# Kernel optimization log

Measured on AMD Instinct MI355X. Metric: run time of the kernel, lower is better.

The kernel has to match this reference:

```python
import jax, jax.numpy as jnp
import numpy as np

B, DV, W, H = 128, 2048, 14, 14
S = W * H            # 196 spatial positions
DQ = 2048            # question vector dim
DA = 1200            # attention dim_v == dim_q == dim_mm (MLB elementwise fusion)
G = 4                # nb_glimpses
DH = 2048            # fusion dim_h (total); per-glimpse = DH // G
NANS = 3000


def setup_inputs() -> dict:
    key = jax.random.key(0)
    ks = jax.random.split(key, 16)
    s = 0.02
    return {
        "input_v": jax.random.normal(ks[0], (B, DV, W, H), jnp.float32),
        "x_q_vec": jax.random.normal(ks[1], (B, DQ), jnp.float32),
        # conv_v_att: 1x1 conv DV->DA  (expressed as channel matmul)
        "Wv_att": jax.random.normal(ks[2], (DV, DA), jnp.float32) * s,
        "bv_att": jnp.zeros((DA,), jnp.float32),
        # linear_q_att: DQ->DA
        "Wq_att": jax.random.normal(ks[3], (DQ, DA), jnp.float32) * s,
        "bq_att": jnp.zeros((DA,), jnp.float32),
        # conv_att: 1x1 conv DA->G
        "Wa": jax.random.normal(ks[4], (DA, G), jnp.float32) * s,
        "ba": jnp.zeros((G,), jnp.float32),
        # per-glimpse fusion linears DV -> DH//G, stacked over glimpses
        "Wf": jax.random.normal(ks[5], (G, DV, DH // G), jnp.float32) * s,
        "bf": jnp.zeros((G, DH // G), jnp.float32),
        # linear_q_fusion: DQ -> DH
        "Wqf": jax.random.normal(ks[6], (DQ, DH), jnp.float32) * s,
        "bqf": jnp.zeros((DH,), jnp.float32),
        # linear_classif: DH -> NANS
        "Wc": jax.random.normal(ks[7], (DH, NANS), jnp.float32) * s,
        "bc": jnp.zeros((NANS,), jnp.float32),
    }


def reference(input_v, x_q_vec, Wv_att, bv_att, Wq_att, bq_att, Wa, ba,
              Wf, bf, Wqf, bqf, Wc, bc):
    b = input_v.shape[0]
    v_flat = input_v.reshape(b, DV, S)                      # [B, DV, S]

    # --- attention scores ---
    # conv_v_att (1x1) + tanh -> [B, S, DA]
    x_v = jnp.tanh(jnp.einsum('bcs,cd->bsd', v_flat, Wv_att) + bv_att)
    # linear_q_att + tanh -> [B, DA], broadcast over spatial
    x_q = jnp.tanh(x_q_vec @ Wq_att + bq_att)
    # MLB fusion_att: elementwise multiply, then tanh (activation_mm)
    x_att = jnp.tanh(x_v * x_q[:, None, :])                 # [B, S, DA]
    scores = jnp.einsum('bsd,dg->bsg', x_att, Wa) + ba      # [B, S, G]
    att = jax.nn.softmax(scores, axis=1)                    # softmax over spatial

    # --- weighted pooling per glimpse ---
    v_att = jnp.einsum('bsg,bcs->bgc', att, v_flat)         # [B, G, DV]

    # --- fusion of glimpses ---
    xv = jnp.tanh(jnp.einsum('bgc,gch->bgh', v_att, Wf) + bf)  # [B, G, DH/G]
    xv = xv.reshape(b, DH)                                   # concat glimpses
    xq = jnp.tanh(x_q_vec @ Wqf + bqf)                       # [B, DH]
    x = xv * xq                                              # MLB fusion_classif

    # --- classifier ---
    x = jnp.tanh(x)
    return x @ Wc + bc                                       # [B, NANS]
```

## Files before the change

### kernel.cpp

```cpp
#include <hip/hip_runtime.h>
#include <hip/hip_bf16.h>

#define BB   128
#define DV   2048
#define SS   196
#define DQ   2048
#define DA   1200
#define DAP  1280
#define GG   4
#define DH   2048
#define NANS 3000
#define NANSP 3008
#define MROWS (BB*SS)
#define NT   5
#define KSPLIT 8
#define KCHUNK (DV/KSPLIT)
#define NQ   (DAP + DH)

typedef __attribute__((ext_vector_type(8))) short bf16x8;
typedef __attribute__((ext_vector_type(4))) float f32x4;

__device__ __forceinline__ float fast_tanh(float x) {
    float e = __expf(2.0f * x);
    return 1.0f - 2.0f * __builtin_amdgcn_rcpf(e + 1.0f);
}

__device__ __forceinline__ void async_copy16(const void* gsrc, void* ldst) {
    __builtin_amdgcn_global_load_lds(
        (const __attribute__((address_space(1))) void*)gsrc,
        (__attribute__((address_space(3))) void*)ldst, 16, 0, 0);
}

__global__ void pad_misc(const float* __restrict__ bv, const float* __restrict__ Wa,
                         float* __restrict__ bvp, float* __restrict__ wap) {
    int i = blockIdx.x * 256 + threadIdx.x;
    if (i < DAP) bvp[i] = (i < DA) ? bv[i] : 0.f;
    if (i < DAP * GG) {
        int d = i >> 2;
        wap[i] = (d < DA) ? Wa[i] : 0.f;
    }
}

__global__ __launch_bounds__(256) void transpose_v(const float* __restrict__ v,
                                                   __hip_bfloat16* __restrict__ vt) {
    const int b    = blockIdx.z;
    const int t    = threadIdx.x;
    const int lane = t & 63;
    const int w    = t >> 6;
    const int sl   = lane >> 2;
    const int cq   = lane & 3;
    const int s    = blockIdx.y * 16 + sl;
    const int c0   = blockIdx.x * 128 + w * 32 + cq * 8;
    if (s >= SS) return;
    const float* src = v + (size_t)b * DV * SS + (size_t)c0 * SS + s;
    float f[8];
#pragma unroll
    for (int i = 0; i < 8; ++i) f[i] = src[(size_t)i * SS];
    union { bf16x8 v8; __hip_bfloat16 h[8]; } u;
#pragma unroll
    for (int i = 0; i < 8; ++i) u.h[i] = __float2bfloat16(f[i]);
    *(bf16x8*)(vt + ((size_t)b * SS + s) * DV + c0) = u.v8;
}

__global__ __launch_bounds__(256) void transpose_w(const float* __restrict__ Wv,
                                                   __hip_bfloat16* __restrict__ wvt) {
    __shared__ float tile[64][65];
    const int d0 = blockIdx.x * 64;
    const int c0 = blockIdx.y * 64;
    const int t  = threadIdx.x;
    const int col  = t & 63;
    const int rowb = t >> 6;
#pragma unroll
    for (int i = 0; i < 16; ++i) {
        int c = rowb + i * 4;
        int d = d0 + col;
        tile[c][col] = (d < DA) ? Wv[(size_t)(c0 + c) * DA + d] : 0.f;
    }
    __syncthreads();
#pragma unroll
    for (int i = 0; i < 16; ++i) {
        int dl = rowb + i * 4;
        wvt[(size_t)(d0 + dl) * DV + c0 + col] = __float2bfloat16(tile[col][dl]);
    }
}

template <int SEL>
__global__ __launch_bounds__(256) void gemm_partial(
    const float* __restrict__ A, int lda,
    const float* __restrict__ Bm, const float* __restrict__ B2,
    float* __restrict__ Cp, int Npad) {
    __shared__ float As[64 * 132];
    __shared__ float Bs[64 * 68];
    const int t     = threadIdx.x;
    const int n0    = blockIdx.x * 64;
    const int kbase = blockIdx.y * KCHUNK;

    const float* Aeff = A;
    const float* Beff;
    int ldb, ncol0, nlim;
    if (SEL == 0) {
        Beff = Bm; ldb = NANS; ncol0 = n0; nlim = NANS;
    } else if (SEL == 1) {
        int gg = n0 >> 9;
        Aeff = A + gg * 2048;
        Beff = Bm + (size_t)gg * 2048 * 512;
        ldb = 512; ncol0 = n0 & 511; nlim = 1 << 30;
    } else {
        if (n0 < DAP) { Beff = Bm; ldb = DA; ncol0 = n0;      nlim = DA; }
        else          { Beff = B2; ldb = DH; ncol0 = n0 - DAP; nlim = 1 << 30; }
    }

    const int tm = (t & 31) * 4;
    const int tn = (t >> 5) * 8;
    float acc[4][8] = {};

    for (int k0 = kbase; k0 < kbase + KCHUNK; k0 += 64) {
        {
            int kk = t & 63, mb = (t >> 6) * 32;
#pragma unroll
            for (int i = 0; i < 32; ++i)
                As[kk * 132 + mb + i] = Aeff[(size_t)(mb + i) * lda + k0 + kk];
        }
        {
            int j = t & 63, kr = t >> 6;
            bool ok = (ncol0 + j) < nlim;
#pragma unroll
            for (int i = 0; i < 16; ++i) {
                int k = kr + i * 4;
                Bs[k * 68 + j] = ok ? Beff[(size_t)(k0 + k) * ldb + ncol0 + j] : 0.f;
            }
        }
        __syncthreads();
#pragma unroll
        for (int kk = 0; kk < 64; ++kk) {
            const float4 av = *(const float4*)(As + kk * 132 + tm);
            const float4 b0 = *(const float4*)(Bs + kk * 68 + tn);
            const float4 b1 = *(const float4*)(Bs + kk * 68 + tn + 4);
            const float am[4] = {av.x, av.y, av.z, av.w};
#pragma unroll
            for (int i = 0; i < 4; ++i) {
                acc[i][0] += am[i] * b0.x; acc[i][1] += am[i] * b0.y;
                acc[i][2] += am[i] * b0.z; acc[i][3] += am[i] * b0.w;
                acc[i][4] += am[i] * b1.x; acc[i][5] += am[i] * b1.y;
                acc[i][6] += am[i] * b1.z; acc[i][7] += am[i] * b1.w;
            }
        }
        __syncthreads();
    }
#pragma unroll
    for (int i = 0; i < 4; ++i) {
        size_t base = ((size_t)blockIdx.y * 128 + tm + i) * Npad + n0 + tn;
        float4 v0 = {acc[i][0], acc[i][1], acc[i][2], acc[i][3]};
        float4 v1 = {acc[i][4], acc[i][5], acc[i][6], acc[i][7]};
        *(float4*)(Cp + base) = v0;
        *(float4*)(Cp + base + 4) = v1;
    }
}

template <int MODE>
__global__ __launch_bounds__(256) void gemm_epilogue(
    const float* __restrict__ Cp, int Npad, int Nreal,
    const float* __restrict__ bias, const float* __restrict__ aux,
    float* __restrict__ out, int ldo) {
    int n = blockIdx.x * 256 + threadIdx.x;
    int m = blockIdx.y;
    if (n >= Npad) return;
    float s = 0.f;
#pragma unroll
    for (int ks = 0; ks < KSPLIT; ++ks)
        s += Cp[((size_t)ks * 128 + m) * Npad + n];
    if (MODE == 0) {
        if (n >= Nreal) return;
        out[(size_t)m * ldo + n] = s + bias[n];
    } else {
        float xv = fast_tanh(s + bias[n]);
        out[(size_t)m * ldo + n] = fast_tanh(xv * aux[(size_t)m * 2048 + n]);
    }
}

__global__ __launch_bounds__(256) void epilogue_q(
    const float* __restrict__ Cp,
    const float* __restrict__ bqa, const float* __restrict__ bqf,
    float* __restrict__ qatt, float* __restrict__ qfus) {
    int n = blockIdx.x * 256 + threadIdx.x;
    int m = blockIdx.y;
    if (n >= NQ) return;
    float s = 0.f;
#pragma unroll
    for (int ks = 0; ks < KSPLIT; ++ks)
        s += Cp[((size_t)ks * 128 + m) * NQ + n];
    if (n < DAP) {
        qatt[(size_t)m * DAP + n] = (n < DA) ? fast_tanh(s + bqa[n]) : 0.f;
    } else {
        int j = n - DAP;
        qfus[(size_t)m * DH + j] = fast_tanh(s + bqf[j]);
    }
}

__global__ __launch_bounds__(512, 2) void big_gemm(
    const __hip_bfloat16* __restrict__ vt,
    const __hip_bfloat16* __restrict__ wt,
    const float* __restrict__ bvp,
    const float* __restrict__ qatt,
    const float* __restrict__ wap,
    float* __restrict__ scores_p) {
    __shared__ __align__(16) char lds[131072];
    __shared__ __align__(16) float wa_s[256 * 4];
    __shared__ float qs[3 * 256];

    const int t    = threadIdx.x;
    const int lane = t & 63;
    const int w    = t >> 6;
    const int wr   = w >> 2;
    const int wc   = w & 3;

    int bid = blockIdx.x;
    int grp = bid / 40, r = bid % 40;
    int mt, nt;
    if (grp < 12) { mt = grp * 8 + (r & 7); nt = r >> 3; }
    else          { mt = 96 + (r & 1);      nt = r >> 1; }
    const int m0 = mt * 256, n0 = nt * 256;
    const int b_lo = m0 / SS;
    const int bs1  = (b_lo + 1) * SS;
    const int bs2  = (b_lo + 2) * SS;

    if (t < 256) *(float4*)(wa_s + t * 4) = *(const float4*)(wap + (n0 + t) * 4);
    {
        int j = t >> 8, c = t & 255;
        int b = b_lo + j;
        qs[t] = (b < BB) ? qatt[(size_t)b * DAP + n0 + c] : 0.f;
        if (t < 256) {
            int b2 = b_lo + 2;
            qs[512 + t] = (b2 < BB) ? qatt[(size_t)b2 * DAP + n0 + t] : 0.f;
        }
    }
    __syncthreads();

    const int srow   = t >> 2;
    const int schunk = (t & 3) ^ ((t >> 3) & 3);
    const __hip_bfloat16* aG = vt + (size_t)(m0 + srow) * DV + schunk * 8;
    const __hip_bfloat16* bG = wt + (size_t)(n0 + srow) * DV + schunk * 8;

    auto STAGE_ITEM = [&](int buf, int k, int p) {
        const int ks = p >> 1, mat = p & 1;
        const __hip_bfloat16* g = (mat ? bG : aG) + (size_t)k * 64 + ks * 32;
        char* dst = lds + buf * 65536 + ks * 32768 + mat * 16384 + t * 16;
        async_copy16(g, dst);
        async_copy16(g + (size_t)128 * DV, dst + 8192);
    };

    const int rchk = ((lane >> 4) ^ (((lane & 15) >> 1) & 3)) * 16;
    const int aRow = (wr * 128 + (lane & 15)) * 64;
    const int bRow = (wc * 64 + (lane & 15)) * 64;

    f32x4 acc[8][4];
#pragma unroll
    for (int i = 0; i < 8; ++i)
#pragma unroll
        for (int j = 0; j < 4; ++j) acc[i][j] = (f32x4){0.f, 0.f, 0.f, 0.f};

    STAGE_ITEM(0, 0, 0); STAGE_ITEM(0, 0, 1);
    STAGE_ITEM(0, 0, 2); STAGE_ITEM(0, 0, 3);
    asm volatile("s_waitcnt vmcnt(4)" ::: "memory");
    __builtin_amdgcn_s_barrier();

    for (int kt = 0; kt < 32; ++kt) {
        const int cur = kt & 1;
        const char* Xb = lds + cur * 65536;
        bf16x8 bfr[4];
#pragma unroll
        for (int p = 0; p < 4; ++p) {
            const int ks = p >> 1, mh = p & 1;
            const char* Ar = Xb + ks * 32768;
            bf16x8 afr[4];
#pragma unroll
            for (int q = 0; q < 4; ++q)
                afr[q] = *(const bf16x8*)(Ar + aRow + (mh * 64 + q * 16) * 64 + rchk);
            if (mh == 0) {
#pragma unroll
                for (int ni = 0; ni < 4; ++ni)
                    bfr[ni] = *(const bf16x8*)(Ar + 16384 + bRow + (ni * 16) * 64 + rchk);
            }
            if (kt < 31) STAGE_ITEM(cur ^ 1, kt + 1, p);
            if (p == 1) {
                if (kt < 31) asm volatile("s_waitcnt vmcnt(4)" ::: "memory");
                else         asm volatile("s_waitcnt vmcnt(0)" ::: "memory");
            } else if (p == 3 && kt < 31) {
                asm volatile("s_waitcnt vmcnt(4)" ::: "memory");
            }
            __builtin_amdgcn_s_barrier();
            __builtin_amdgcn_s_setprio(1);
#pragma unroll
            for (int q = 0; q < 4; ++q)
#pragma unroll
                for (int ni = 0; ni < 4; ++ni)
                    acc[mh * 4 + q][ni] = __builtin_amdgcn_mfma_f32_16x16x32_bf16(
                        afr[q], bfr[ni], acc[mh * 4 + q][ni], 0, 0, 0);
            __builtin_amdgcn_s_setprio(0);
        }
    }

    __syncthreads();
    float* sc = (float*)lds;

    const int colb_l = wc * 64 + (lane & 15);
    const int colb_g = n0 + colb_l;
    float bvv[4];
    float4 wv[4];
#pragma unroll
    for (int ni = 0; ni < 4; ++ni) {
        bvv[ni] = bvp[colb_g + ni * 16];
        wv[ni]  = *(const float4*)(wa_s + (colb_l + ni * 16) * 4);
    }
#pragma unroll
    for (int mi = 0; mi < 8; ++mi) {
#pragma unroll
        for (int rr = 0; rr < 4; ++rr) {
            int lrow = wr * 128 + mi * 16 + ((lane >> 4) << 2) + rr;
            int row  = m0 + lrow;
            int qoff = (row >= bs1 ? 256 : 0) + (row >= bs2 ? 256 : 0);
            float p0 = 0.f, p1 = 0.f, p2 = 0.f, p3 = 0.f;
#pragma unroll
            for (int ni = 0; ni < 4; ++ni) {
                float xv = fast_tanh(acc[mi][ni][rr] + bvv[ni]);
                float xa = fast_tanh(xv * qs[qoff + colb_l + ni * 16]);
                p0 += xa * wv[ni].x; p1 += xa * wv[ni].y;
                p2 += xa * wv[ni].z; p3 += xa * wv[ni].w;
            }
#pragma unroll
            for (int mk = 1; mk < 16; mk <<= 1) {
                p0 += __shfl_xor(p0, mk); p1 += __shfl_xor(p1, mk);
                p2 += __shfl_xor(p2, mk); p3 += __shfl_xor(p3, mk);
            }
            if ((lane & 15) == 0)
                *(float4*)(sc + ((size_t)wc * 256 + lrow) * 4) =
                    (float4){p0, p1, p2, p3};
        }
    }
    __syncthreads();
    if (t < 256) {
        float4 s0 = *(float4*)(sc + (0 * 256 + t) * 4);
        float4 s1 = *(float4*)(sc + (1 * 256 + t) * 4);
        float4 s2 = *(float4*)(sc + (2 * 256 + t) * 4);
        float4 s3 = *(float4*)(sc + (3 * 256 + t) * 4);
        float4 s = {s0.x + s1.x + s2.x + s3.x, s0.y + s1.y + s2.y + s3.y,
                    s0.z + s1.z + s2.z + s3.z, s0.w + s1.w + s2.w + s3.w};
        *(float4*)(scores_p + ((size_t)nt * MROWS + m0 + t) * 4) = s;
    }
}

__global__ __launch_bounds__(256) void softmax_pool(
    const float* __restrict__ scores_p,
    const __hip_bfloat16* __restrict__ vt,
    float* __restrict__ vatt) {
    __shared__ __align__(16) float att[SS * GG];
    const int b = blockIdx.y;
    const int t = threadIdx.x;
    if (t < SS) {
        float4 s = {0.f, 0.f, 0.f, 0.f};
#pragma unroll
        for (int ntile = 0; ntile < NT; ++ntile) {
            float4 p = *(const float4*)(scores_p + ((size_t)ntile * MROWS + b * SS + t) * 4);
            s.x += p.x; s.y += p.y; s.z += p.z; s.w += p.w;
        }
        *(float4*)(att + t * 4) = s;
    }
    __syncthreads();
    {
        const int g = t >> 6;
        const int lane = t & 63;
        float mx = -3.0e38f;
        for (int s = lane; s < SS; s += 64) mx = fmaxf(mx, att[s * 4 + g]);
#pragma unroll
        for (int m = 32; m > 0; m >>= 1) mx = fmaxf(mx, __shfl_xor(mx, m));
        float sum = 0.f;
        for (int s = lane; s < SS; s += 64) sum += __expf(att[s * 4 + g] - mx);
#pragma unroll
        for (int m = 32; m > 0; m >>= 1) sum += __shfl_xor(sum, m);
        float inv = __builtin_amdgcn_rcpf(sum);
        for (int s = lane; s < SS; s += 64) att[s * 4 + g] = __expf(att[s * 4 + g] - mx) * inv;
    }
    __syncthreads();
    const int c = blockIdx.x * 512 + t * 2;
    const __hip_bfloat16* vp = vt + (size_t)b * SS * DV + c;
    float a00 = 0, a01 = 0, a02 = 0, a03 = 0;
    float a10 = 0, a11 = 0, a12 = 0, a13 = 0;
#pragma unroll 4
    for (int s = 0; s < SS; ++s) {
        unsigned u = *(const unsigned*)(vp + (size_t)s * DV);
        float v0 = __uint_as_float(u << 16);
        float v1 = __uint_as_float(u & 0xffff0000u);
        float4 aw = *(const float4*)(att + s * 4);
        a00 += v0 * aw.x; a01 += v0 * aw.y; a02 += v0 * aw.z; a03 += v0 * aw.w;
        a10 += v1 * aw.x; a11 += v1 * aw.y; a12 += v1 * aw.z; a13 += v1 * aw.w;
    }
    float* vb = vatt + (size_t)b * GG * DV;
    vb[0 * DV + c] = a00; vb[0 * DV + c + 1] = a10;
    vb[1 * DV + c] = a01; vb[1 * DV + c + 1] = a11;
    vb[2 * DV + c] = a02; vb[2 * DV + c + 1] = a12;
    vb[3 * DV + c] = a03; vb[3 * DV + c + 1] = a13;
}

extern "C" void kernel_launch(void* const* d_in, const int* in_sizes, int n_in,
                              void* d_out, int out_size, void* d_ws, size_t ws_size,
                              hipStream_t stream) {
    const float* input_v = (const float*)d_in[0];
    const float* x_q     = (const float*)d_in[1];
    const float* Wv      = (const float*)d_in[2];
    const float* bv      = (const float*)d_in[3];
    const float* Wq_att  = (const float*)d_in[4];
    const float* bq_att  = (const float*)d_in[5];
    const float* Wa      = (const float*)d_in[6];
    const float* Wf      = (const float*)d_in[8];
    const float* bf_     = (const float*)d_in[9];
    const float* Wqf     = (const float*)d_in[10];
    const float* bqf     = (const float*)d_in[11];
    const float* Wc      = (const float*)d_in[12];
    const float* bc      = (const float*)d_in[13];
    float* out = (float*)d_out;

    char* wsb = (char*)d_ws;
    size_t off = 0;
    auto carve = [&](size_t bytes) -> void* {
        void* p = wsb + off;
        off += (bytes + 255) & ~(size_t)255;
        return p;
    };
    __hip_bfloat16* vt  = (__hip_bfloat16*)carve((size_t)MROWS * DV * 2);
    __hip_bfloat16* wvt = (__hip_bfloat16*)carve((size_t)DAP * DV * 2);
    float* Cp       = (float*)carve((size_t)KSPLIT * 128 * NQ * 4);
    float* scores_p = (float*)carve((size_t)NT * MROWS * GG * 4);
    float* qatt = (float*)carve((size_t)BB * DAP * 4);
    float* qfus = (float*)carve((size_t)BB * DH * 4);
    float* bvp  = (float*)carve((size_t)DAP * 4);
    float* wap  = (float*)carve((size_t)DAP * GG * 4);
    float* vatt = (float*)carve((size_t)BB * GG * DV * 4);
    float* xbuf = (float*)carve((size_t)BB * DH * 4);
    (void)ws_size; (void)n_in; (void)in_sizes; (void)out_size;

    pad_misc<<<dim3(20), 256, 0, stream>>>(bv, Wa, bvp, wap);
    transpose_v<<<dim3(DV / 128, 13, BB), 256, 0, stream>>>(input_v, vt);
    transpose_w<<<dim3(DAP / 64, DV / 64), 256, 0, stream>>>(Wv, wvt);

    gemm_partial<2><<<dim3(NQ / 64, KSPLIT), 256, 0, stream>>>(
        x_q, DQ, Wq_att, Wqf, Cp, NQ);
    epilogue_q<<<dim3(NQ / 256, BB), 256, 0, stream>>>(Cp, bq_att, bqf, qatt, qfus);

    big_gemm<<<dim3(490), 512, 0, stream>>>(vt, wvt, bvp, qatt, wap, scores_p);

    softmax_pool<<<dim3(4, BB), 256, 0, stream>>>(scores_p, vt, vatt);

    gemm_partial<1><<<dim3(DH / 64, KSPLIT), 256, 0, stream>>>(
        vatt, GG * DV, Wf, nullptr, Cp, DH);
    gemm_epilogue<2><<<dim3(DH / 256, BB), 256, 0, stream>>>(
        Cp, DH, DH, bf_, qfus, xbuf, DH);

    gemm_partial<0><<<dim3(NANSP / 64, KSPLIT), 256, 0, stream>>>(
        xbuf, DH, Wc, nullptr, Cp, NANSP);
    gemm_epilogue<0><<<dim3(NANSP / 256 + 1, BB), 256, 0, stream>>>(
        Cp, NANSP, NANS, bc, nullptr, out, NANS);
}
```

Baseline: 646.0 us.

## Restructure big GEMM k-loop to two barriers per tile; widen pooling loads

The main GEMM inner loop now works through two k-substeps per tile instead of four phases. Each substep issues two staging loads up front, loads B fragments once, and runs two MFMA batches over the M halves. This halves the number of barriers and waitcnts per k-tile, with a sched_barrier to order the second A-fragment load. Separately, the softmax/pooling kernel has each thread handle four channels with 8-byte loads and float4 stores, on half as many blocks, which reduces parallelism in that kernel.

```diff
diff --git a/kernel.cpp b/kernel.cpp
--- a/kernel.cpp
+++ b/kernel.cpp
@@ -267,36 +267,44 @@
     for (int kt = 0; kt < 32; ++kt) {
         const int cur = kt & 1;
         const char* Xb = lds + cur * 65536;
-        bf16x8 bfr[4];
-#pragma unroll
-        for (int p = 0; p < 4; ++p) {
-            const int ks = p >> 1, mh = p & 1;
+#pragma unroll
+        for (int ks = 0; ks < 2; ++ks) {
             const char* Ar = Xb + ks * 32768;
-            bf16x8 afr[4];
+            if (kt < 31) {
+                STAGE_ITEM(cur ^ 1, kt + 1, 2 * ks);
+                STAGE_ITEM(cur ^ 1, kt + 1, 2 * ks + 1);
+            }
+            bf16x8 bfr[4], afr[4];
+#pragma unroll
+            for (int ni = 0; ni < 4; ++ni)
+                bfr[ni] = *(const bf16x8*)(Ar + 16384 + bRow + (ni * 16) * 64 + rchk);
 #pragma unroll
             for (int q = 0; q < 4; ++q)
-                afr[q] = *(const bf16x8*)(Ar + aRow + (mh * 64 + q * 16) * 64 + rchk);
-            if (mh == 0) {
+                afr[q] = *(const bf16x8*)(Ar + aRow + (q * 16) * 64 + rchk);
+            __builtin_amdgcn_s_setprio(1);
+#pragma unroll
+            for (int q = 0; q < 4; ++q)
 #pragma unroll
                 for (int ni = 0; ni < 4; ++ni)
-                    bfr[ni] = *(const bf16x8*)(Ar + 16384 + bRow + (ni * 16) * 64 + rchk);
-            }
-            if (kt < 31) STAGE_ITEM(cur ^ 1, kt + 1, p);
-            if (p == 1) {
-                if (kt < 31) asm volatile("s_waitcnt vmcnt(4)" ::: "memory");
-                else         asm volatile("s_waitcnt vmcnt(0)" ::: "memory");
-            } else if (p == 3 && kt < 31) {
-                asm volatile("s_waitcnt vmcnt(4)" ::: "memory");
-            }
+                    acc[q][ni] = __builtin_amdgcn_mfma_f32_16x16x32_bf16(
+                        afr[q], bfr[ni], acc[q][ni], 0, 0, 0);
+            __builtin_amdgcn_s_setprio(0);
+            __builtin_amdgcn_sched_barrier(0x8);
+            bf16x8 af2[4];
+#pragma unroll
+            for (int q = 0; q < 4; ++q)
+                af2[q] = *(const bf16x8*)(Ar + aRow + ((4 + q) * 16) * 64 + rchk);
+            __builtin_amdgcn_s_setprio(1);
+#pragma unroll
+            for (int q = 0; q < 4; ++q)
+#pragma unroll
+                for (int ni = 0; ni < 4; ++ni)
+                    acc[4 + q][ni] = __builtin_amdgcn_mfma_f32_16x16x32_bf16(
+                        af2[q], bfr[ni], acc[4 + q][ni], 0, 0, 0);
+            __builtin_amdgcn_s_setprio(0);
+            if (kt < 31) asm volatile("s_waitcnt vmcnt(4)" ::: "memory");
+            else         asm volatile("s_waitcnt vmcnt(0)" ::: "memory");
             __builtin_amdgcn_s_barrier();
-            __builtin_amdgcn_s_setprio(1);
-#pragma unroll
-            for (int q = 0; q < 4; ++q)
-#pragma unroll
-                for (int ni = 0; ni < 4; ++ni)
-                    acc[mh * 4 + q][ni] = __builtin_amdgcn_mfma_f32_16x16x32_bf16(
-                        afr[q], bfr[ni], acc[mh * 4 + q][ni], 0, 0, 0);
-            __builtin_amdgcn_s_setprio(0);
         }
     }
 
@@ -381,24 +389,28 @@
         for (int s = lane; s < SS; s += 64) att[s * 4 + g] = __expf(att[s * 4 + g] - mx) * inv;
     }
     __syncthreads();
-    const int c = blockIdx.x * 512 + t * 2;
+    const int c = blockIdx.x * 1024 + t * 4;
     const __hip_bfloat16* vp = vt + (size_t)b * SS * DV + c;
-    float a00 = 0, a01 = 0, a02 = 0, a03 = 0;
-    float a10 = 0, a11 = 0, a12 = 0, a13 = 0;
+    float a0[4] = {}, a1[4] = {}, a2[4] = {}, a3[4] = {};
 #pragma unroll 4
     for (int s = 0; s < SS; ++s) {
-        unsigned u = *(const unsigned*)(vp + (size_t)s * DV);
-        float v0 = __uint_as_float(u << 16);
-        float v1 = __uint_as_float(u & 0xffff0000u);
+        uint2 u = *(const uint2*)(vp + (size_t)s * DV);
+        float v0 = __uint_as_float(u.x << 16);
+        float v1 = __uint_as_float(u.x & 0xffff0000u);
+        float v2 = __uint_as_float(u.y << 16);
+        float v3 = __uint_as_float(u.y & 0xffff0000u);
         float4 aw = *(const float4*)(att + s * 4);
-        a00 += v0 * aw.x; a01 += v0 * aw.y; a02 += v0 * aw.z; a03 += v0 * aw.w;
-        a10 += v1 * aw.x; a11 += v1 * aw.y; a12 += v1 * aw.z; a13 += v1 * aw.w;
+        a0[0] += v0 * aw.x; a0[1] += v0 * aw.y; a0[2] += v0 * aw.z; a0[3] += v0 * aw.w;
+        a1[0] += v1 * aw.x; a1[1] += v1 * aw.y; a1[2] += v1 * aw.z; a1[3] += v1 * aw.w;
+        a2[0] += v2 * aw.x; a2[1] += v2 * aw.y; a2[2] += v2 * aw.z; a2[3] += v2 * aw.w;
+        a3[0] += v3 * aw.x; a3[1] += v3 * aw.y; a3[2] += v3 * aw.z; a3[3] += v3 * aw.w;
     }
     float* vb = vatt + (size_t)b * GG * DV;
-    vb[0 * DV + c] = a00; vb[0 * DV + c + 1] = a10;
-    vb[1 * DV + c] = a01; vb[1 * DV + c + 1] = a11;
-    vb[2 * DV + c] = a02; vb[2 * DV + c + 1] = a12;
-    vb[3 * DV + c] = a03; vb[3 * DV + c + 1] = a13;
+#pragma unroll
+    for (int g = 0; g < GG; ++g) {
+        float4 o = {a0[g], a1[g], a2[g], a3[g]};
+        *(float4*)(vb + (size_t)g * DV + c) = o;
+    }
 }
 
 extern "C" void kernel_launch(void* const* d_in, const int* in_sizes, int n_in,
@@ -448,7 +460,7 @@
 
     big_gemm<<<dim3(490), 512, 0, stream>>>(vt, wvt, bvp, qatt, wap, scores_p);
 
-    softmax_pool<<<dim3(4, BB), 256, 0, stream>>>(scores_p, vt, vatt);
+    softmax_pool<<<dim3(2, BB), 256, 0, stream>>>(scores_p, vt, vatt);
 
     gemm_partial<1><<<dim3(DH / 64, KSPLIT), 256, 0, stream>>>(
         vatt, GG * DV, Wf, nullptr, Cp, DH);
```

Measured after the change: 672.3 us. 4.1% more time.
